# Kernel tuning notes

Hardware: AMD Instinct MI355X
Metric: run time of the kernel (lower is better)

## Reference

```python
import jax, jax.numpy as jnp
import numpy as np

D_MODEL = 1024
N_HEAD = 16
D_H = D_MODEL // N_HEAD


def setup_inputs() -> dict:
    key = jax.random.key(0)
    ks = jax.random.split(key, 5)
    scale = 1.0 / np.sqrt(D_MODEL)
    x = jax.random.normal(ks[0], (4, 2048, D_MODEL), dtype=jnp.float32)
    # torch nn.Linear weights: shape (out_features, in_features)
    W_qkv = jax.random.uniform(ks[1], (3 * D_MODEL, D_MODEL), dtype=jnp.float32, minval=-scale, maxval=scale)
    b_qkv = jax.random.uniform(ks[2], (3 * D_MODEL,), dtype=jnp.float32, minval=-scale, maxval=scale)
    W_o = jax.random.uniform(ks[3], (D_MODEL, D_MODEL), dtype=jnp.float32, minval=-scale, maxval=scale)
    b_o = jax.random.uniform(ks[4], (D_MODEL,), dtype=jnp.float32, minval=-scale, maxval=scale)
    return {"x": x, "W_qkv": W_qkv, "b_qkv": b_qkv, "W_o": W_o, "b_o": b_o}


def reference(x, W_qkv, b_qkv, W_o, b_o):
    B, S, D = x.shape
    qkv = jnp.einsum('bsd,ed->bse', x, W_qkv) + b_qkv  # [B,S,3D]
    q, k, v = jnp.split(qkv, 3, axis=-1)
    # [B,H,S,d_h]
    q = q.reshape(B, S, N_HEAD, D_H).transpose(0, 2, 1, 3)
    k = k.reshape(B, S, N_HEAD, D_H).transpose(0, 2, 1, 3)
    v = v.reshape(B, S, N_HEAD, D_H).transpose(0, 2, 1, 3)
    sim = jnp.einsum('bhqd,bhkd->bhqk', q, k) / jnp.sqrt(jnp.float32(D_H))
    neg_inf = jnp.finfo(sim.dtype).min
    causal = jnp.tril(jnp.ones((S, S), dtype=bool))
    sim = jnp.where(causal[None, None], sim, neg_inf)
    attn = jax.nn.softmax(sim, axis=-1)
    out = jnp.einsum('bhqk,bhkd->bhqd', attn, v)  # [B,H,S,d_h]
    out = out.transpose(0, 2, 1, 3).reshape(B, S, D)
    return jnp.einsum('bsd,ed->bse', out, W_o) + b_o
```

## Files before the change

kernel.cpp:

```cpp
#include <hip/hip_runtime.h>

#define D_MODEL 1024
#define S_LEN   2048
#define BATCH   4
#define NH      16
#define DH      64
#define M_ROWS  (BATCH * S_LEN)

typedef __attribute__((ext_vector_type(8))) short short8;
typedef __attribute__((ext_vector_type(4))) float floatx4;
typedef unsigned short ushort_t;
typedef __attribute__((ext_vector_type(4))) ushort_t ushortx4;

__device__ __forceinline__ ushort_t f2bf(float f) {
    union { float f; unsigned u; } v; v.f = f;
    unsigned r = v.u + 0x7FFFu + ((v.u >> 16) & 1u);
    return (ushort_t)(r >> 16);
}

__device__ __forceinline__ int pack2(float lo, float hi) {
    return (int)__builtin_amdgcn_perm(__float_as_uint(hi), __float_as_uint(lo), 0x07060302u);
}

__device__ __forceinline__ void async_copy16(const ushort_t* g, ushort_t* l) {
    __builtin_amdgcn_global_load_lds(
        (const __attribute__((address_space(1))) void*)g,
        (__attribute__((address_space(3))) void*)l,
        16, 0, 0);
}

#define N0 (M_ROWS * D_MODEL)
#define N1 (3 * D_MODEL * D_MODEL)
#define N2 (D_MODEL * D_MODEL)
#define NQUADS ((N0 + N1 + N2) / 4)

__global__ __launch_bounds__(256)
void cvt_f32_bf16(const float* __restrict__ s0, const float* __restrict__ s1,
                  const float* __restrict__ s2, ushort_t* __restrict__ d0,
                  ushort_t* __restrict__ d1, ushort_t* __restrict__ d2)
{
    const int q = blockIdx.x * 256 + threadIdx.x;
    if (q >= NQUADS) return;
    const float* s; ushort_t* d; int e;
    if (q < N0 / 4)            { s = s0; d = d0; e = q * 4; }
    else if (q < (N0 + N1) / 4){ s = s1; d = d1; e = q * 4 - N0; }
    else                       { s = s2; d = d2; e = q * 4 - N0 - N1; }
    const float4 v = *(const float4*)&s[e];
    ushortx4 o;
    o[0] = f2bf(v.x); o[1] = f2bf(v.y); o[2] = f2bf(v.z); o[3] = f2bf(v.w);
    *(ushortx4*)&d[e] = o;
}

template<bool F32OUT, bool VSPLIT>
__global__ __launch_bounds__(256)
void gemm_bt_bias(const ushort_t* __restrict__ A, const ushort_t* __restrict__ B,
                  const float* __restrict__ bias, void* __restrict__ Cv,
                  ushort_t* __restrict__ vt, int M, int N, int K)
{
    constexpr int BK = 64;
    constexpr float C2 = 0.18033688011112042f;
    __shared__ ushort_t As[128][BK];
    __shared__ ushort_t Bs[128][BK];

    const int tid  = threadIdx.x;
    const int lane = tid & 63;
    const int wave = tid >> 6;
    const int quad = lane >> 4;
    const int l16  = lane & 15;
    const int bm   = blockIdx.y * 128;
    const int bn   = blockIdx.x * 128;
    const int wm   = (wave & 1) * 64;
    const int wn   = (wave >> 1) * 64;

    floatx4 acc[4][4] = {};

    const int l8r = lane >> 3;
    const int c8  = lane & 7;
    const int swz = l16 & 7;

    for (int k0 = 0; k0 < K; k0 += BK) {
        __syncthreads();
        #pragma unroll
        for (int i = wave; i < 16; i += 4) {
            const int row = i * 8 + l8r;
            const int cc  = (c8 ^ l8r) * 8;
            async_copy16(&A[(size_t)(bm + row) * K + k0 + cc], &As[i * 8][0]);
            async_copy16(&B[(size_t)(bn + row) * K + k0 + cc], &Bs[i * 8][0]);
        }
        __syncthreads();

        #pragma unroll
        for (int h = 0; h < 2; h++) {
            short8 af[4], bfr[4];
            #pragma unroll
            for (int i = 0; i < 4; i++)
                af[i]  = *(const short8*)&As[wm + i * 16 + l16][((h * 4 + quad) ^ swz) * 8];
            #pragma unroll
            for (int i = 0; i < 4; i++)
                bfr[i] = *(const short8*)&Bs[wn + i * 16 + l16][((h * 4 + quad) ^ swz) * 8];

            #pragma unroll
            for (int mi = 0; mi < 4; mi++)
                #pragma unroll
                for (int ni = 0; ni < 4; ni++)
                    acc[mi][ni] = __builtin_amdgcn_mfma_f32_16x16x32_bf16(af[mi], bfr[ni], acc[mi][ni], 0, 0, 0);
        }
    }

    #pragma unroll
    for (int ni = 0; ni < 4; ni++) {
        const int col = bn + wn + ni * 16 + l16;
        const float bv = bias[col];
        #pragma unroll
        for (int mi = 0; mi < 4; mi++)
            #pragma unroll
            for (int r = 0; r < 4; r++) {
                const int row = bm + wm + mi * 16 + quad * 4 + r;
                const float val = acc[mi][ni][r] + bv;
                if (VSPLIT) {
                    if (col < 2 * D_MODEL) {
                        const float vv = (col < D_MODEL) ? val * C2 : val;
                        ((ushort_t*)Cv)[(size_t)row * 2048 + col] = f2bf(vv);
                    } else {
                        const int vcol = col - 2 * D_MODEL;
                        const int h = vcol >> 6, dh = vcol & 63;
                        const int b = row >> 11, s = row & 2047;
                        const int sp = (s & ~63) | ((s & 15) << 2) | ((s >> 4) & 3);
                        vt[(((size_t)(b * NH + h)) * DH + dh) * S_LEN + sp] = f2bf(val);
                    }
                } else if (F32OUT) {
                    ((float*)Cv)[(size_t)row * N + col] = val;
                } else {
                    ((ushort_t*)Cv)[(size_t)row * N + col] = f2bf(val);
                }
            }
    }
}

#define BKV 64

struct TileState {
    short8  qf[2];
    floatx4 o[4];
    float   l[4];
};

__device__ __forceinline__ void attn_tile(
    const ushort_t (*__restrict__ Ks)[DH], const ushort_t (*__restrict__ Vs)[BKV],
    ushort_t* __restrict__ Psw, TileState& st, bool diag,
    int wave, int quad, int l16, int swz, short8 ones)
{
    floatx4 sc[4];
    #pragma unroll
    for (int ns = 0; ns < 4; ns++) {
        const short8 kf0 = *(const short8*)&Ks[ns * 16 + l16][(quad ^ swz) * 8];
        const short8 kf1 = *(const short8*)&Ks[ns * 16 + l16][((4 + quad) ^ swz) * 8];
        floatx4 z = {};
        z = __builtin_amdgcn_mfma_f32_16x16x32_bf16(st.qf[0], kf0, z, 0, 0, 0);
        z = __builtin_amdgcn_mfma_f32_16x16x32_bf16(st.qf[1], kf1, z, 0, 0, 0);
        sc[ns] = z;
    }

    #pragma unroll
    for (int r = 0; r < 4; r++) {
        const int qloc = wave * 16 + quad * 4 + r;
        float p[4];
        #pragma unroll
        for (int ns = 0; ns < 4; ns++) {
            float v = sc[ns][r];
            if (diag) {
                const int kj = ns * 16 + l16;
                v = (kj <= qloc) ? v : -1e30f;
            }
            p[ns] = __builtin_amdgcn_exp2f(v);
        }
        int2 w;
        w.x = pack2(p[0], p[1]);
        w.y = pack2(p[2], p[3]);
        const int row = quad * 4 + r;
        *(int2*)((char*)Psw + row * 128 + (((l16 >> 1) ^ (row & 7)) << 4) + ((l16 & 1) << 3)) = w;
    }

    short8 pf[2];
    #pragma unroll
    for (int c = 0; c < 2; c++)
        pf[c] = *(const short8*)((const char*)Psw + l16 * 128 + ((((c << 2) | quad) ^ (l16 & 7)) << 4));

    floatx4 racc = {};
    racc = __builtin_amdgcn_mfma_f32_16x16x32_bf16(pf[0], ones, racc, 0, 0, 0);
    racc = __builtin_amdgcn_mfma_f32_16x16x32_bf16(pf[1], ones, racc, 0, 0, 0);

    #pragma unroll
    for (int r = 0; r < 4; r++)
        st.l[r] += racc[r];

    #pragma unroll
    for (int d = 0; d < 4; d++) {
        #pragma unroll
        for (int c = 0; c < 2; c++) {
            const short8 vf = *(const short8*)&Vs[d * 16 + l16][((c * 4 + quad) ^ swz) * 8];
            st.o[d] = __builtin_amdgcn_mfma_f32_16x16x32_bf16(pf[c], vf, st.o[d], 0, 0, 0);
        }
    }
}

__device__ __forceinline__ void stage_tile(
    const ushort_t* __restrict__ kg, const ushort_t* __restrict__ vg, int kb,
    ushort_t (*__restrict__ Ksb)[DH], ushort_t (*__restrict__ Vsb)[BKV],
    int wave, int l8r, int c8)
{
    #pragma unroll
    for (int i = wave; i < 8; i += 4) {
        const int row = i * 8 + l8r;
        const int cc  = (c8 ^ l8r) * 8;
        async_copy16(&kg[(size_t)(kb + row) * 2048 + cc], &Ksb[i * 8][0]);
        async_copy16(&vg[(size_t)row * S_LEN + kb + cc], &Vsb[i * 8][0]);
    }
}

__global__ __launch_bounds__(256, 4)
void attn_causal(const ushort_t* __restrict__ qk, const ushort_t* __restrict__ vt,
                 ushort_t* __restrict__ out)
{
    __shared__ ushort_t Ks[2][BKV][DH];
    __shared__ ushort_t Vs[2][DH][BKV];
    __shared__ ushort_t Ps[4][16][64];

    const int tid  = threadIdx.x;
    const int lane = tid & 63;
    const int wave = tid >> 6;
    const int quad = lane >> 4;
    const int l16  = lane & 15;
    const int l8r  = lane >> 3;
    const int c8   = lane & 7;
    const int swz  = l16 & 7;

    const int qa = blockIdx.x;
    const int qb = 31 - qa;
    const int bh = blockIdx.y;
    const int b  = bh >> 4;
    const int h  = bh & 15;

    const size_t qkbase = (size_t)b * S_LEN * 2048;
    const ushort_t* kg = qk + qkbase + D_MODEL + h * DH;
    const ushort_t* vg = vt + (size_t)(b * NH + h) * DH * S_LEN;

    TileState sa, sb;
    #pragma unroll
    for (int r = 0; r < 4; r++) { sa.l[r] = 0.f; sb.l[r] = 0.f; }
    #pragma unroll
    for (int d = 0; d < 4; d++) { sa.o[d] = (floatx4){}; sb.o[d] = (floatx4){}; }

    {
        const ushort_t* qpa = qk + qkbase + (size_t)(qa * 64 + wave * 16 + l16) * 2048 + h * DH;
        sa.qf[0] = *(const short8*)(qpa + quad * 8);
        sa.qf[1] = *(const short8*)(qpa + 32 + quad * 8);
        const ushort_t* qpb = qk + qkbase + (size_t)(qb * 64 + wave * 16 + l16) * 2048 + h * DH;
        sb.qf[0] = *(const short8*)(qpb + quad * 8);
        sb.qf[1] = *(const short8*)(qpb + 32 + quad * 8);
    }

    short8 ones;
    #pragma unroll
    for (int j = 0; j < 8; j++) ones[j] = (short)0x3F80;

    stage_tile(kg, vg, 0, Ks[0], Vs[0], wave, l8r, c8);

    int cur = 0;
    for (int t = 0; t <= qb; t++) {
        __syncthreads();
        if (t < qb)
            stage_tile(kg, vg, (t + 1) * BKV, Ks[cur ^ 1], Vs[cur ^ 1], wave, l8r, c8);

        if (t <= qa) attn_tile(Ks[cur], Vs[cur], &Ps[wave][0][0], sa, t == qa, wave, quad, l16, swz, ones);
        attn_tile(Ks[cur], Vs[cur], &Ps[wave][0][0], sb, t == qb, wave, quad, l16, swz, ones);
        cur ^= 1;
    }

    #pragma unroll
    for (int r = 0; r < 4; r++) {
        const float inva = 1.0f / sa.l[r];
        const float invb = 1.0f / sb.l[r];
        const int ra = qa * 64 + wave * 16 + quad * 4 + r;
        const int rb = qb * 64 + wave * 16 + quad * 4 + r;
        #pragma unroll
        for (int d = 0; d < 4; d++) {
            out[(size_t)(b * S_LEN + ra) * D_MODEL + h * DH + d * 16 + l16] = f2bf(sa.o[d][r] * inva);
            out[(size_t)(b * S_LEN + rb) * D_MODEL + h * DH + d * 16 + l16] = f2bf(sb.o[d][r] * invb);
        }
    }
}

extern "C" void kernel_launch(void* const* d_in, const int* in_sizes, int n_in,
                              void* d_out, int out_size, void* d_ws, size_t ws_size,
                              hipStream_t stream)
{
    const float* x    = (const float*)d_in[0];
    const float* Wqkv = (const float*)d_in[1];
    const float* bqkv = (const float*)d_in[2];
    const float* Wo   = (const float*)d_in[3];
    const float* bo   = (const float*)d_in[4];
    float* out = (float*)d_out;

    ushort_t* xb    = (ushort_t*)d_ws;
    ushort_t* wqkvb = xb + N0;
    ushort_t* wob   = wqkvb + N1;
    ushort_t* qkbuf = wob + N2;
    ushort_t* vtbuf = qkbuf + (size_t)M_ROWS * 2048;
    ushort_t* att   = vtbuf + (size_t)BATCH * NH * DH * S_LEN;

    dim3 blk(256);
    cvt_f32_bf16<<<dim3((NQUADS + 255) / 256), blk, 0, stream>>>(x, Wqkv, Wo, xb, wqkvb, wob);
    gemm_bt_bias<false, true><<<dim3((3 * D_MODEL) / 128, M_ROWS / 128), blk, 0, stream>>>(
        xb, wqkvb, bqkv, qkbuf, vtbuf, M_ROWS, 3 * D_MODEL, D_MODEL);
    attn_causal<<<dim3(16, BATCH * NH), blk, 0, stream>>>(qkbuf, vtbuf, att);
    gemm_bt_bias<true, false><<<dim3(D_MODEL / 128, M_ROWS / 128), blk, 0, stream>>>(
        att, wob, bo, out, nullptr, M_ROWS, D_MODEL, D_MODEL);
}
```

Measured before the change: 264.1 us.

## Double-buffer LDS and enlarge GEMM tile to 256x128 with 512 threads

The projection GEMM now uses a 256x128 block tile with 8 waves, so each B tile staged in LDS is reused across twice as many rows. LDS is double-buffered: the next K-slice is issued asynchronously while MFMAs run on the current one, and one of the two barriers per iteration is removed. The aim is to hide global-load latency and cut redundant B traffic. In exchange, LDS use per block roughly doubles, which limits how many blocks fit on a CU, and the output-projection grid has fewer blocks.

```diff
diff --git a/kernel.cpp b/kernel.cpp
--- a/kernel.cpp
+++ b/kernel.cpp
@@ -51,53 +51,70 @@
     *(ushortx4*)&d[e] = o;
 }
 
+template<int R>
+__device__ __forceinline__ void stage_ab(
+    const ushort_t* __restrict__ G, int grow0, int K, int k0,
+    ushort_t (*__restrict__ S)[64], int wave, int l8r, int c8)
+{
+    #pragma unroll
+    for (int i = 0; i < R / 64; i++) {
+        const int row = i * 64 + wave * 8 + l8r;
+        const int cc  = (c8 ^ l8r) * 8;
+        async_copy16(&G[(size_t)(grow0 + row) * K + k0 + cc], &S[i * 64 + wave * 8][0]);
+    }
+}
+
 template<bool F32OUT, bool VSPLIT>
-__global__ __launch_bounds__(256)
+__global__ __launch_bounds__(512, 2)
 void gemm_bt_bias(const ushort_t* __restrict__ A, const ushort_t* __restrict__ B,
                   const float* __restrict__ bias, void* __restrict__ Cv,
                   ushort_t* __restrict__ vt, int M, int N, int K)
 {
+    constexpr int BM = 256;
+    constexpr int BN = 128;
     constexpr int BK = 64;
     constexpr float C2 = 0.18033688011112042f;
-    __shared__ ushort_t As[128][BK];
-    __shared__ ushort_t Bs[128][BK];
+    __shared__ ushort_t As[2][BM][BK];
+    __shared__ ushort_t Bs[2][BN][BK];
 
     const int tid  = threadIdx.x;
     const int lane = tid & 63;
     const int wave = tid >> 6;
     const int quad = lane >> 4;
     const int l16  = lane & 15;
-    const int bm   = blockIdx.y * 128;
-    const int bn   = blockIdx.x * 128;
-    const int wm   = (wave & 1) * 64;
-    const int wn   = (wave >> 1) * 64;
+    const int l8r  = lane >> 3;
+    const int c8   = lane & 7;
+    const int swz  = l16 & 7;
+    const int bm   = blockIdx.y * BM;
+    const int bn   = blockIdx.x * BN;
+    const int wm   = (wave & 3) * 64;
+    const int wn   = (wave >> 2) * 64;
 
     floatx4 acc[4][4] = {};
 
-    const int l8r = lane >> 3;
-    const int c8  = lane & 7;
-    const int swz = l16 & 7;
-
+    stage_ab<BM>(A, bm, K, 0, As[0], wave, l8r, c8);
+    stage_ab<BN>(B, bn, K, 0, Bs[0], wave, l8r, c8);
+
+    int buf = 0;
     for (int k0 = 0; k0 < K; k0 += BK) {
         __syncthreads();
-        #pragma unroll
-        for (int i = wave; i < 16; i += 4) {
-            const int row = i * 8 + l8r;
-            const int cc  = (c8 ^ l8r) * 8;
-            async_copy16(&A[(size_t)(bm + row) * K + k0 + cc], &As[i * 8][0]);
-            async_copy16(&B[(size_t)(bn + row) * K + k0 + cc], &Bs[i * 8][0]);
-        }
-        __syncthreads();
+        if (k0 + BK < K) {
+            stage_ab<BM>(A, bm, K, k0 + BK, As[buf ^ 1], wave, l8r, c8);
+            stage_ab<BN>(B, bn, K, k0 + BK, Bs[buf ^ 1], wave, l8r, c8);
+        }
+
+        const ushort_t (*__restrict__ Asb)[BK] = As[buf];
+        const ushort_t (*__restrict__ Bsb)[BK] = Bs[buf];
 
         #pragma unroll
         for (int h = 0; h < 2; h++) {
             short8 af[4], bfr[4];
             #pragma unroll
             for (int i = 0; i < 4; i++)
-                af[i]  = *(const short8*)&As[wm + i * 16 + l16][((h * 4 + quad) ^ swz) * 8];
+                af[i]  = *(const short8*)&Asb[wm + i * 16 + l16][((h * 4 + quad) ^ swz) * 8];
             #pragma unroll
             for (int i = 0; i < 4; i++)
-                bfr[i] = *(const short8*)&Bs[wn + i * 16 + l16][((h * 4 + quad) ^ swz) * 8];
+                bfr[i] = *(const short8*)&Bsb[wn + i * 16 + l16][((h * 4 + quad) ^ swz) * 8];
 
             #pragma unroll
             for (int mi = 0; mi < 4; mi++)
@@ -105,6 +122,7 @@
                 for (int ni = 0; ni < 4; ni++)
                     acc[mi][ni] = __builtin_amdgcn_mfma_f32_16x16x32_bf16(af[mi], bfr[ni], acc[mi][ni], 0, 0, 0);
         }
+        buf ^= 1;
     }
 
     #pragma unroll
@@ -309,11 +327,10 @@
     ushort_t* vtbuf = qkbuf + (size_t)M_ROWS * 2048;
     ushort_t* att   = vtbuf + (size_t)BATCH * NH * DH * S_LEN;
 
-    dim3 blk(256);
-    cvt_f32_bf16<<<dim3((NQUADS + 255) / 256), blk, 0, stream>>>(x, Wqkv, Wo, xb, wqkvb, wob);
-    gemm_bt_bias<false, true><<<dim3((3 * D_MODEL) / 128, M_ROWS / 128), blk, 0, stream>>>(
+    cvt_f32_bf16<<<dim3((NQUADS + 255) / 256), dim3(256), 0, stream>>>(x, Wqkv, Wo, xb, wqkvb, wob);
+    gemm_bt_bias<false, true><<<dim3((3 * D_MODEL) / 128, M_ROWS / 256), dim3(512), 0, stream>>>(
         xb, wqkvb, bqkv, qkbuf, vtbuf, M_ROWS, 3 * D_MODEL, D_MODEL);
-    attn_causal<<<dim3(16, BATCH * NH), blk, 0, stream>>>(qkbuf, vtbuf, att);
-    gemm_bt_bias<true, false><<<dim3(D_MODEL / 128, M_ROWS / 128), blk, 0, stream>>>(
+    attn_causal<<<dim3(16, BATCH * NH), dim3(256), 0, stream>>>(qkbuf, vtbuf, att);
+    gemm_bt_bias<true, false><<<dim3(D_MODEL / 128, M_ROWS / 256), dim3(512), 0, stream>>>(
         att, wob, bo, out, nullptr, M_ROWS, D_MODEL, D_MODEL);
 }
```

New measurement: 296.2 us. 1.12x slower.

## Template GEMM tile sizes, use 256x128 tiles for QKV and swizzle block order

Applied to the files above, without the earlier changes.

The GEMM kernel takes its block tile size, wave count and occupancy hint as template parameters. The QKV projection now runs 512-thread blocks over 256x128 tiles, so each B tile is reused across more rows. Block indices are remapped with a stride-8 swizzle so that blocks scheduled together cover different tiles, likely to improve L2 or XCD locality. Global and LDS load pointers are precomputed outside the k loop. The larger tile raises LDS use per block and may reduce the number of resident blocks.

```diff
diff --git a/kernel.cpp b/kernel.cpp
--- a/kernel.cpp
+++ b/kernel.cpp
@@ -51,42 +51,61 @@
     *(ushortx4*)&d[e] = o;
 }
 
-template<bool F32OUT, bool VSPLIT>
-__global__ __launch_bounds__(256)
+template<int BM, int BN, int NWAVES, int MINW, bool F32OUT, bool VSPLIT>
+__global__ __launch_bounds__(NWAVES * 64, MINW)
 void gemm_bt_bias(const ushort_t* __restrict__ A, const ushort_t* __restrict__ B,
                   const float* __restrict__ bias, void* __restrict__ Cv,
                   ushort_t* __restrict__ vt, int M, int N, int K)
 {
     constexpr int BK = 64;
+    constexpr int AI = BM / 8 / NWAVES;
+    constexpr int BI = BN / 8 / NWAVES;
     constexpr float C2 = 0.18033688011112042f;
-    __shared__ ushort_t As[128][BK];
-    __shared__ ushort_t Bs[128][BK];
+    __shared__ ushort_t As[BM][BK];
+    __shared__ ushort_t Bs[BN][BK];
 
     const int tid  = threadIdx.x;
     const int lane = tid & 63;
     const int wave = tid >> 6;
     const int quad = lane >> 4;
     const int l16  = lane & 15;
-    const int bm   = blockIdx.y * 128;
-    const int bn   = blockIdx.x * 128;
-    const int wm   = (wave & 1) * 64;
-    const int wn   = (wave >> 1) * 64;
+    const int l8r  = lane >> 3;
+    const int c8   = lane & 7;
+    const int swz  = l16 & 7;
+
+    const int gdx = gridDim.x;
+    const int bid = blockIdx.y * gdx + blockIdx.x;
+    const int nwg = gdx * gridDim.y;
+    const int sw  = (bid & 7) * (nwg >> 3) + (bid >> 3);
+    const int bm  = (sw / gdx) * BM;
+    const int bn  = (sw % gdx) * BN;
+
+    const int wm = (wave % (BM / 64)) * 64;
+    const int wn = (wave / (BM / 64)) * 64;
+
+    const ushort_t* ag[AI]; ushort_t* al[AI];
+    const ushort_t* bg[BI]; ushort_t* bl[BI];
+    #pragma unroll
+    for (int i = 0; i < AI; i++) {
+        const int ri = (wave + i * NWAVES) * 8;
+        ag[i] = &A[(size_t)(bm + ri + l8r) * K + (c8 ^ l8r) * 8];
+        al[i] = &As[ri][0];
+    }
+    #pragma unroll
+    for (int i = 0; i < BI; i++) {
+        const int ri = (wave + i * NWAVES) * 8;
+        bg[i] = &B[(size_t)(bn + ri + l8r) * K + (c8 ^ l8r) * 8];
+        bl[i] = &Bs[ri][0];
+    }
 
     floatx4 acc[4][4] = {};
-
-    const int l8r = lane >> 3;
-    const int c8  = lane & 7;
-    const int swz = l16 & 7;
 
     for (int k0 = 0; k0 < K; k0 += BK) {
         __syncthreads();
         #pragma unroll
-        for (int i = wave; i < 16; i += 4) {
-            const int row = i * 8 + l8r;
-            const int cc  = (c8 ^ l8r) * 8;
-            async_copy16(&A[(size_t)(bm + row) * K + k0 + cc], &As[i * 8][0]);
-            async_copy16(&B[(size_t)(bn + row) * K + k0 + cc], &Bs[i * 8][0]);
-        }
+        for (int i = 0; i < AI; i++) async_copy16(ag[i] + k0, al[i]);
+        #pragma unroll
+        for (int i = 0; i < BI; i++) async_copy16(bg[i] + k0, bl[i]);
         __syncthreads();
 
         #pragma unroll
@@ -309,11 +328,12 @@
     ushort_t* vtbuf = qkbuf + (size_t)M_ROWS * 2048;
     ushort_t* att   = vtbuf + (size_t)BATCH * NH * DH * S_LEN;
 
-    dim3 blk(256);
-    cvt_f32_bf16<<<dim3((NQUADS + 255) / 256), blk, 0, stream>>>(x, Wqkv, Wo, xb, wqkvb, wob);
-    gemm_bt_bias<false, true><<<dim3((3 * D_MODEL) / 128, M_ROWS / 128), blk, 0, stream>>>(
+    cvt_f32_bf16<<<dim3((NQUADS + 255) / 256), dim3(256), 0, stream>>>(x, Wqkv, Wo, xb, wqkvb, wob);
+    gemm_bt_bias<256, 128, 8, 6, false, true>
+        <<<dim3((3 * D_MODEL) / 128, M_ROWS / 256), dim3(512), 0, stream>>>(
         xb, wqkvb, bqkv, qkbuf, vtbuf, M_ROWS, 3 * D_MODEL, D_MODEL);
-    attn_causal<<<dim3(16, BATCH * NH), blk, 0, stream>>>(qkbuf, vtbuf, att);
-    gemm_bt_bias<true, false><<<dim3(D_MODEL / 128, M_ROWS / 128), blk, 0, stream>>>(
+    attn_causal<<<dim3(16, BATCH * NH), dim3(256), 0, stream>>>(qkbuf, vtbuf, att);
+    gemm_bt_bias<128, 128, 4, 2, true, false>
+        <<<dim3(D_MODEL / 128, M_ROWS / 128), dim3(256), 0, stream>>>(
         att, wob, bo, out, nullptr, M_ROWS, D_MODEL, D_MODEL);
 }
```

New measurement: 653.1 us. 147% more time.
